# Optimization experiments

Measured on AMD Instinct MI355X. Metric: run time of the kernel, lower is better.

Reference implementation:

```python
import jax, jax.numpy as jnp
import numpy as np

B, T, C, H, DFF = 4, 1024, 1024, 16, 4096
HS = C // H  # 64
EPS = 1e-5


def layer_norm(x, g, b):
    mu = jnp.mean(x, axis=-1, keepdims=True)
    var = jnp.var(x, axis=-1, keepdims=True)
    return (x - mu) * jax.lax.rsqrt(var + EPS) * g + b


def setup_inputs() -> dict:
    key = jax.random.key(0)
    ks = jax.random.split(key, 12)
    s = 0.02
    return {
        "x": jax.random.normal(ks[0], (B, T, C), jnp.float32),
        "wq": jax.random.normal(ks[1], (H, C, HS), jnp.float32) * s,
        "wk": jax.random.normal(ks[2], (H, C, HS), jnp.float32) * s,
        "wv": jax.random.normal(ks[3], (H, C, HS), jnp.float32) * s,
        "w_proj": jax.random.normal(ks[4], (H * HS, C), jnp.float32) * s,
        "b_proj": jnp.zeros((C,), jnp.float32),
        "w1": jax.random.normal(ks[5], (C, DFF), jnp.float32) * s,
        "b1": jnp.zeros((DFF,), jnp.float32),
        "w2": jax.random.normal(ks[6], (DFF, C), jnp.float32) * s,
        "b2": jnp.zeros((C,), jnp.float32),
        "g1": jnp.ones((C,), jnp.float32),
        "be1": jnp.zeros((C,), jnp.float32),
        "g2": jnp.ones((C,), jnp.float32),
        "be2": jnp.zeros((C,), jnp.float32),
    }


def reference(x, wq, wk, wv, w_proj, b_proj, w1, b1, w2, b2, g1, be1, g2, be2):
    h = layer_norm(x, g1, be1)
    # per-head projections, vectorized over heads: [B,H,T,HS]
    q = jnp.einsum('btc,hcd->bhtd', h, wq)
    k = jnp.einsum('btc,hcd->bhtd', h, wk)
    v = jnp.einsum('btc,hcd->bhtd', h, wv)
    # mask=None in the original forward, so no causal masking
    wei = jnp.einsum('bhtd,bhsd->bhts', q, k) * (HS ** -0.5)
    wei = jax.nn.softmax(wei, axis=-1)  # [B,H,T,T]
    out = jnp.einsum('bhts,bhsd->bhtd', wei, v)
    out = out.transpose(0, 2, 1, 3).reshape(B, T, H * HS)  # concat heads
    attn_out = out @ w_proj + b_proj
    x = x + attn_out
    h2 = layer_norm(x, g2, be2)
    ff = jax.nn.relu(h2 @ w1 + b1) @ w2 + b2
    x = x + ff
    return x, wei
```

## Files before the change

kernel.cpp:

```cpp
#include <hip/hip_runtime.h>
#include <hip/hip_bf16.h>

#define BB    4
#define TT    1024
#define CC    1024
#define HH    16
#define HSZ   64
#define DFF   4096
#define NTOK  (BB*TT)
#define BHN   (BB*HH)

typedef __attribute__((ext_vector_type(8))) short bf16x8;
typedef __attribute__((ext_vector_type(4))) float f32x4;

__device__ __forceinline__ ushort f2b(float v) {
    union { float f; unsigned u; } c; c.f = v;
    unsigned r = c.u + 0x7fffu + ((c.u >> 16) & 1u);
    return (ushort)(r >> 16);
}
__device__ __forceinline__ void stv(float* p, float v)  { *p = v; }
__device__ __forceinline__ void stv(ushort* p, float v) { *p = f2b(v); }

__device__ __forceinline__ void gload16(const void* g, void* l) {
    __builtin_amdgcn_global_load_lds(
        (const __attribute__((address_space(1))) void*)g,
        (__attribute__((address_space(3))) void*)l, 16, 0, 0);
}

__global__ __launch_bounds__(256)
void ln_k(const float* __restrict__ x, const float* __restrict__ g,
          const float* __restrict__ be, ushort* __restrict__ o)
{
    __shared__ float s1[4], s2[4];
    long row = blockIdx.x;
    const float4* xr = (const float4*)(x + row * CC);
    float4 v = xr[threadIdx.x];
    float a = v.x + v.y + v.z + v.w;
    float b = v.x*v.x + v.y*v.y + v.z*v.z + v.w*v.w;
    for (int off = 32; off > 0; off >>= 1) {
        a += __shfl_down(a, off);
        b += __shfl_down(b, off);
    }
    if ((threadIdx.x & 63) == 0) { s1[threadIdx.x >> 6] = a; s2[threadIdx.x >> 6] = b; }
    __syncthreads();
    float sum = s1[0] + s1[1] + s1[2] + s1[3];
    float sq  = s2[0] + s2[1] + s2[2] + s2[3];
    float mu  = sum * (1.0f / CC);
    float var = sq * (1.0f / CC) - mu * mu;
    float inv = rsqrtf(var + 1e-5f);
    float4 gg = ((const float4*)g)[threadIdx.x];
    float4 bb = ((const float4*)be)[threadIdx.x];
    ushort4 r;
    r.x = f2b((v.x - mu) * inv * gg.x + bb.x);
    r.y = f2b((v.y - mu) * inv * gg.y + bb.y);
    r.z = f2b((v.z - mu) * inv * gg.z + bb.z);
    r.w = f2b((v.w - mu) * inv * gg.w + bb.w);
    ((ushort4*)(o + row * CC))[threadIdx.x] = r;
}

__global__ __launch_bounds__(256)
void tcvt_k(const float* __restrict__ src, ushort* __restrict__ dst, int R, int Cc)
{
    __shared__ float t[32][33];
    const long bz = blockIdx.z;
    src += bz * (long)R * Cc;
    dst += bz * (long)R * Cc;
    int r0 = blockIdx.y * 32, c0 = blockIdx.x * 32;
    int tx = threadIdx.x & 31, ty = threadIdx.x >> 5;
#pragma unroll
    for (int i = 0; i < 4; i++)
        t[ty + 8*i][tx] = src[(long)(r0 + ty + 8*i) * Cc + c0 + tx];
    __syncthreads();
#pragma unroll
    for (int i = 0; i < 4; i++)
        dst[(long)(c0 + ty + 8*i) * R + r0 + tx] = f2b(t[tx][ty + 8*i]);
}

enum { OL_PLAIN = 0, OL_QKV3 = 1 };
constexpr int EBIAS = 1, ERELU = 2, ERES = 4, ESCALE = 8;

template<int BM, int BN, int WM, int WN, int OL, int EPI, typename OutT>
__global__ __launch_bounds__(256)
void mgemm_k(const ushort* __restrict__ A, const ushort* __restrict__ Bt,
             const float* __restrict__ bias, const float* __restrict__ res,
             OutT* __restrict__ C, int M, int N, int K,
             long sA, long sB, long sC, float scale)
{
    constexpr int BK = 64;
    constexpr int FM = BM / WM / 16, FN = BN / WN / 16;
    __shared__ ushort As[BM * BK];
    __shared__ ushort Bs[BN * BK];
    const int tid = threadIdx.x;
    const int w = tid >> 6, l = tid & 63;
    const int wr = w / WN, wc = w % WN;
    const int l15 = l & 15, l4 = l >> 4;
    const int bh = blockIdx.z;
    const ushort* Ap = A  + (long)bh * sA + (long)(blockIdx.y * BM) * K;
    const ushort* Bp = Bt + (long)bh * sB + (long)(blockIdx.x * BN) * K;

    f32x4 acc[FM][FN];
#pragma unroll
    for (int m = 0; m < FM; m++)
#pragma unroll
        for (int n = 0; n < FN; n++) acc[m][n] = (f32x4){0.f, 0.f, 0.f, 0.f};

    const int arow = tid >> 3;
    const int achk = tid & 7;

    for (int k0 = 0; k0 < K; k0 += BK) {
#pragma unroll
        for (int i = 0; i < BM / 32; i++)
            gload16(Ap + (long)(i*32 + arow) * K + k0 + achk*8,
                    &As[(i*32 + w*8) * BK]);
#pragma unroll
        for (int i = 0; i < BN / 32; i++)
            gload16(Bp + (long)(i*32 + arow) * K + k0 + achk*8,
                    &Bs[(i*32 + w*8) * BK]);
        __syncthreads();
#pragma unroll
        for (int kk = 0; kk < 2; kk++) {
            const int ko = kk*32 + l4*8;
            bf16x8 af[FM], bfr[FN];
#pragma unroll
            for (int m = 0; m < FM; m++)
                af[m] = *(const bf16x8*)&As[(wr*(BM/WM) + m*16 + l15) * BK + ko];
#pragma unroll
            for (int n = 0; n < FN; n++)
                bfr[n] = *(const bf16x8*)&Bs[(wc*(BN/WN) + n*16 + l15) * BK + ko];
#pragma unroll
            for (int m = 0; m < FM; m++)
#pragma unroll
                for (int n = 0; n < FN; n++)
                    acc[m][n] = __builtin_amdgcn_mfma_f32_16x16x32_bf16(
                        af[m], bfr[n], acc[m][n], 0, 0, 0);
        }
        __syncthreads();
    }

#pragma unroll
    for (int m = 0; m < FM; m++) {
        int rbase = blockIdx.y*BM + wr*(BM/WM) + m*16 + l4*4;
#pragma unroll
        for (int n = 0; n < FN; n++) {
            int col = blockIdx.x*BN + wc*(BN/WN) + n*16 + l15;
#pragma unroll
            for (int r = 0; r < 4; r++) {
                int row = rbase + r;
                float v = acc[m][n][r];
                if (EPI & ESCALE) v *= scale;
                if (EPI & EBIAS)  v += bias[col];
                if (EPI & ERELU)  v = fmaxf(v, 0.f);
                if (EPI & ERES)   v += res[(long)row * N + col];
                long idx;
                if (OL == OL_PLAIN) {
                    idx = (long)row * N + col;
                } else {
                    int seg = col >> 10;
                    int cl  = col & 1023;
                    long bh_ = ((long)((row >> 10) * HH + (cl >> 6))) * 65536;
                    long off = (seg == 2)
                        ? bh_ + (long)(cl & 63) * 1024 + (row & 1023)
                        : bh_ + (long)(row & 1023) * 64 + (cl & 63);
                    idx = (long)seg * (4L << 20) + off;
                }
                stv(&C[(long)bh * sC + idx], v);
            }
        }
    }
}

__global__ __launch_bounds__(256, 2)
void fattn_k(const ushort* __restrict__ q_, const ushort* __restrict__ k_,
             const ushort* __restrict__ vt, float* __restrict__ wei,
             ushort* __restrict__ attn)
{
    __shared__ ushort Qs[128*64];
    __shared__ ushort Ks[128*64];
    __shared__ ushort Vs[64*128];
    __shared__ ushort Ps[128*128];
    float* sred = (float*)Ps;

    const int tid = threadIdx.x;
    const int w = tid >> 6, l = tid & 63;
    const int wr = w >> 1, wc = w & 1;
    const int l15 = l & 15, l4 = l >> 4;
    const int bh = blockIdx.y;
    const int q0 = blockIdx.x * 128;
    const int arow = tid >> 3, achk = tid & 7;

    const ushort* Qp = q_ + (long)bh * 65536;
    const ushort* Kp = k_ + (long)bh * 65536;
    const ushort* Vp = vt + (long)bh * 65536;

#pragma unroll
    for (int i = 0; i < 4; i++)
        gload16(Qp + (long)(q0 + i*32 + arow) * 64 + achk*8, &Qs[(i*32 + w*8)*64]);

    float ssum[4][4];
#pragma unroll
    for (int m = 0; m < 4; m++)
#pragma unroll
        for (int r = 0; r < 4; r++) ssum[m][r] = 0.f;

    for (int st = 0; st < 8; ++st) {
#pragma unroll
        for (int i = 0; i < 4; i++)
            gload16(Kp + (long)(st*128 + i*32 + arow) * 64 + achk*8,
                    &Ks[(i*32 + w*8)*64]);
        __syncthreads();

        f32x4 sacc[4][4];
#pragma unroll
        for (int m = 0; m < 4; m++)
#pragma unroll
            for (int n = 0; n < 4; n++) sacc[m][n] = (f32x4){0.f,0.f,0.f,0.f};
#pragma unroll
        for (int kk = 0; kk < 2; kk++) {
            const int ko = kk*32 + l4*8;
            bf16x8 af[4], bfr[4];
#pragma unroll
            for (int m = 0; m < 4; m++)
                af[m] = *(const bf16x8*)&Qs[(wr*64 + m*16 + l15)*64 + ko];
#pragma unroll
            for (int n = 0; n < 4; n++)
                bfr[n] = *(const bf16x8*)&Ks[(wc*64 + n*16 + l15)*64 + ko];
#pragma unroll
            for (int m = 0; m < 4; m++)
#pragma unroll
                for (int n = 0; n < 4; n++)
                    sacc[m][n] = __builtin_amdgcn_mfma_f32_16x16x32_bf16(
                        af[m], bfr[n], sacc[m][n], 0, 0, 0);
        }
#pragma unroll
        for (int m = 0; m < 4; m++)
#pragma unroll
            for (int r = 0; r < 4; r++) {
                float s = 0.f;
#pragma unroll
                for (int n = 0; n < 4; n++) s += __expf(sacc[m][n][r] * 0.125f);
                ssum[m][r] += s;
            }
        __syncthreads();
    }

    float linv[4][4];
#pragma unroll
    for (int m = 0; m < 4; m++)
#pragma unroll
        for (int r = 0; r < 4; r++) {
            float s = ssum[m][r];
#pragma unroll
            for (int d = 1; d < 16; d <<= 1) s += __shfl_xor(s, d);
            ssum[m][r] = s;
            if (l15 == 0) sred[wc*128 + wr*64 + m*16 + l4*4 + r] = s;
        }
    __syncthreads();
#pragma unroll
    for (int m = 0; m < 4; m++)
#pragma unroll
        for (int r = 0; r < 4; r++) {
            int rg = wr*64 + m*16 + l4*4 + r;
            linv[m][r] = 1.0f / (sred[rg] + sred[128 + rg]);
        }

    f32x4 oacc[4][2];
#pragma unroll
    for (int m = 0; m < 4; m++)
#pragma unroll
        for (int n = 0; n < 2; n++) oacc[m][n] = (f32x4){0.f,0.f,0.f,0.f};

    for (int st = 0; st < 8; ++st) {
#pragma unroll
        for (int i = 0; i < 4; i++)
            gload16(Kp + (long)(st*128 + i*32 + arow) * 64 + achk*8,
                    &Ks[(i*32 + w*8)*64]);
#pragma unroll
        for (int i = 0; i < 4; i++)
            gload16(Vp + (long)(i*16 + (tid>>4)) * 1024 + st*128 + (tid&15)*8,
                    &Vs[(i*16 + w*4)*128]);
        __syncthreads();

        f32x4 sacc[4][4];
#pragma unroll
        for (int m = 0; m < 4; m++)
#pragma unroll
            for (int n = 0; n < 4; n++) sacc[m][n] = (f32x4){0.f,0.f,0.f,0.f};
#pragma unroll
        for (int kk = 0; kk < 2; kk++) {
            const int ko = kk*32 + l4*8;
            bf16x8 af[4], bfr[4];
#pragma unroll
            for (int m = 0; m < 4; m++)
                af[m] = *(const bf16x8*)&Qs[(wr*64 + m*16 + l15)*64 + ko];
#pragma unroll
            for (int n = 0; n < 4; n++)
                bfr[n] = *(const bf16x8*)&Ks[(wc*64 + n*16 + l15)*64 + ko];
#pragma unroll
            for (int m = 0; m < 4; m++)
#pragma unroll
                for (int n = 0; n < 4; n++)
                    sacc[m][n] = __builtin_amdgcn_mfma_f32_16x16x32_bf16(
                        af[m], bfr[n], sacc[m][n], 0, 0, 0);
        }

        float* wrow = wei + (long)bh * (TT*(long)TT) + st*128;
#pragma unroll
        for (int m = 0; m < 4; m++)
#pragma unroll
            for (int r = 0; r < 4; r++) {
                int rg = wr*64 + m*16 + l4*4 + r;
                float li = linv[m][r];
#pragma unroll
                for (int n = 0; n < 4; n++) {
                    int col = wc*64 + n*16 + l15;
                    float p = __expf(sacc[m][n][r] * 0.125f) * li;
                    __builtin_nontemporal_store(p, &wrow[(long)(q0 + rg) * TT + col]);
                    Ps[rg*128 + col] = f2b(p);
                }
            }
        __syncthreads();

#pragma unroll
        for (int kc = 0; kc < 4; ++kc) {
            const int ko = kc*32 + l4*8;
            bf16x8 pa[4], vb[2];
#pragma unroll
            for (int m = 0; m < 4; m++)
                pa[m] = *(const bf16x8*)&Ps[(wr*64 + m*16 + l15)*128 + ko];
#pragma unroll
            for (int n = 0; n < 2; n++)
                vb[n] = *(const bf16x8*)&Vs[(wc*32 + n*16 + l15)*128 + ko];
#pragma unroll
            for (int m = 0; m < 4; m++)
#pragma unroll
                for (int n = 0; n < 2; n++)
                    oacc[m][n] = __builtin_amdgcn_mfma_f32_16x16x32_bf16(
                        pa[m], vb[n], oacc[m][n], 0, 0, 0);
        }
        __syncthreads();
    }

#pragma unroll
    for (int m = 0; m < 4; m++)
#pragma unroll
        for (int r = 0; r < 4; r++) {
            int rg = wr*64 + m*16 + l4*4 + r;
            long rowbase = ((long)(bh >> 4) * TT + q0 + rg) * CC + (long)(bh & 15) * HSZ;
#pragma unroll
            for (int n = 0; n < 2; n++)
                attn[rowbase + wc*32 + n*16 + l15] = f2b(oacc[m][n][r]);
        }
}

extern "C" void kernel_launch(void* const* d_in, const int* in_sizes, int n_in,
                              void* d_out, int out_size, void* d_ws, size_t ws_size,
                              hipStream_t stream)
{
    const float* x      = (const float*)d_in[0];
    const float* wq     = (const float*)d_in[1];
    const float* wk     = (const float*)d_in[2];
    const float* wv     = (const float*)d_in[3];
    const float* w_proj = (const float*)d_in[4];
    const float* b_proj = (const float*)d_in[5];
    const float* w1     = (const float*)d_in[6];
    const float* b1     = (const float*)d_in[7];
    const float* w2     = (const float*)d_in[8];
    const float* b2     = (const float*)d_in[9];
    const float* g1     = (const float*)d_in[10];
    const float* be1    = (const float*)d_in[11];
    const float* g2     = (const float*)d_in[12];
    const float* be2    = (const float*)d_in[13];

    float* out_x = (float*)d_out;
    float* wei   = out_x + (long)NTOK * CC;

    const long MEL = 1 << 20;
    ushort* ws16 = (ushort*)d_ws;
    ushort* h    = ws16;
    ushort* q_   = ws16 + 4*MEL;
    ushort* k_   = ws16 + 8*MEL;
    ushort* vt   = ws16 + 12*MEL;
    ushort* attn = ws16 + 16*MEL;
    ushort* h2   = ws16 + 20*MEL;
    ushort* a1   = ws16 + 24*MEL;
    ushort* wqkvT= ws16 + 40*MEL;
    ushort* w1T  = ws16 + 44*MEL;
    ushort* wpT  = ws16 + 48*MEL;
    ushort* w2T  = ws16 + 49*MEL;
    float*  x1   = (float*)(ws16 + 54*MEL);

    tcvt_k<<<dim3(2, 32, 16),  256, 0, stream>>>(wq,     wqkvT,           1024, 64);
    tcvt_k<<<dim3(2, 32, 16),  256, 0, stream>>>(wk,     wqkvT + 1*MEL,   1024, 64);
    tcvt_k<<<dim3(2, 32, 16),  256, 0, stream>>>(wv,     wqkvT + 2*MEL,   1024, 64);
    tcvt_k<<<dim3(32, 32, 1),  256, 0, stream>>>(w_proj, wpT, 1024, 1024);
    tcvt_k<<<dim3(128, 32, 1), 256, 0, stream>>>(w1,     w1T, 1024, 4096);
    tcvt_k<<<dim3(32, 128, 1), 256, 0, stream>>>(w2,     w2T, 4096, 1024);

    ln_k<<<NTOK, 256, 0, stream>>>(x, g1, be1, h);

    mgemm_k<128,128,2,2,OL_QKV3,0,ushort><<<dim3(24,32,1), 256, 0, stream>>>(
        h, wqkvT, nullptr, nullptr, q_, NTOK, 3072, CC, 0,0,0, 0.f);

    fattn_k<<<dim3(8, 64), 256, 0, stream>>>(q_, k_, vt, wei, attn);

    mgemm_k<128,128,2,2,OL_PLAIN,EBIAS|ERES,float><<<dim3(8,32,1), 256, 0, stream>>>(
        attn, wpT, b_proj, x, x1, NTOK, CC, CC, 0,0,0, 0.f);

    ln_k<<<NTOK, 256, 0, stream>>>(x1, g2, be2, h2);

    mgemm_k<128,128,2,2,OL_PLAIN,EBIAS|ERELU,ushort><<<dim3(32,32,1), 256, 0, stream>>>(
        h2, w1T, b1, nullptr, a1, NTOK, DFF, CC, 0,0,0, 0.f);

    mgemm_k<128,128,2,2,OL_PLAIN,EBIAS|ERES,float><<<dim3(8,32,1), 256, 0, stream>>>(
        a1, w2T, b2, x1, out_x, NTOK, CC, DFF, 0,0,0, 0.f);
}
```

Baseline: 393.7 us.

## Swizzle attention LDS tiles, add MFMA priority hints, merge weight conversions

Applies XOR swizzles to the Q, K, V and P shared-memory tiles in the attention kernel so the 16-byte MFMA fragment reads avoid LDS bank conflicts. It also raises wave priority around the MFMA loops and adds a barrier before P overwrites the reduction scratch. Separately, the six weight transpose/convert launches are merged into one kernel to cut launch overhead. The swizzle indexing must line up between the global-load writes and the fragment reads, which adds a risk of getting it wrong.

```diff
diff --git a/kernel.cpp b/kernel.cpp
--- a/kernel.cpp
+++ b/kernel.cpp
@@ -59,13 +59,32 @@
 }
 
 __global__ __launch_bounds__(256)
-void tcvt_k(const float* __restrict__ src, ushort* __restrict__ dst, int R, int Cc)
+void cvtall_k(const float* __restrict__ wq, const float* __restrict__ wk,
+              const float* __restrict__ wv, const float* __restrict__ wproj,
+              const float* __restrict__ w1, const float* __restrict__ w2,
+              ushort* __restrict__ wqkvT, ushort* __restrict__ wpT,
+              ushort* __restrict__ w1T, ushort* __restrict__ w2T)
 {
     __shared__ float t[32][33];
-    const long bz = blockIdx.z;
-    src += bz * (long)R * Cc;
-    dst += bz * (long)R * Cc;
-    int r0 = blockIdx.y * 32, c0 = blockIdx.x * 32;
+    int idx = blockIdx.x;
+    const float* src; ushort* dst; int R, Cc, bx, by;
+    if (idx < 3072) {
+        int seg = idx >> 10, rem = idx & 1023;
+        int z = rem >> 6, tt2 = rem & 63;
+        src = (seg == 0 ? wq : seg == 1 ? wk : wv) + (long)z * 65536;
+        dst = wqkvT + (long)seg * (1L << 20) + (long)z * 65536;
+        R = 1024; Cc = 64; bx = tt2 & 1; by = tt2 >> 1;
+    } else if (idx < 4096) {
+        int tt2 = idx - 3072;
+        src = wproj; dst = wpT; R = 1024; Cc = 1024; bx = tt2 & 31; by = tt2 >> 5;
+    } else if (idx < 8192) {
+        int tt2 = idx - 4096;
+        src = w1; dst = w1T; R = 1024; Cc = 4096; bx = tt2 & 127; by = tt2 >> 7;
+    } else {
+        int tt2 = idx - 8192;
+        src = w2; dst = w2T; R = 4096; Cc = 1024; bx = tt2 & 31; by = tt2 >> 5;
+    }
+    int r0 = by * 32, c0 = bx * 32;
     int tx = threadIdx.x & 31, ty = threadIdx.x >> 5;
 #pragma unroll
     for (int i = 0; i < 4; i++)
@@ -187,6 +206,11 @@
     const int bh = blockIdx.y;
     const int q0 = blockIdx.x * 128;
     const int arow = tid >> 3, achk = tid & 7;
+    const int kchk = achk ^ (arow & 7);
+    const int vrow = tid >> 4;
+    const int vchk = (tid & 15) ^ (vrow & 15);
+    const int sw8  = (l15 & 7) << 3;
+    const int sw16 = l15 << 3;
 
     const ushort* Qp = q_ + (long)bh * 65536;
     const ushort* Kp = k_ + (long)bh * 65536;
@@ -194,7 +218,7 @@
 
 #pragma unroll
     for (int i = 0; i < 4; i++)
-        gload16(Qp + (long)(q0 + i*32 + arow) * 64 + achk*8, &Qs[(i*32 + w*8)*64]);
+        gload16(Qp + (long)(q0 + i*32 + arow) * 64 + kchk*8, &Qs[(i*32 + w*8)*64]);
 
     float ssum[4][4];
 #pragma unroll
@@ -205,7 +229,7 @@
     for (int st = 0; st < 8; ++st) {
 #pragma unroll
         for (int i = 0; i < 4; i++)
-            gload16(Kp + (long)(st*128 + i*32 + arow) * 64 + achk*8,
+            gload16(Kp + (long)(st*128 + i*32 + arow) * 64 + kchk*8,
                     &Ks[(i*32 + w*8)*64]);
         __syncthreads();
 
@@ -214,16 +238,17 @@
         for (int m = 0; m < 4; m++)
 #pragma unroll
             for (int n = 0; n < 4; n++) sacc[m][n] = (f32x4){0.f,0.f,0.f,0.f};
+        __builtin_amdgcn_s_setprio(1);
 #pragma unroll
         for (int kk = 0; kk < 2; kk++) {
             const int ko = kk*32 + l4*8;
             bf16x8 af[4], bfr[4];
 #pragma unroll
             for (int m = 0; m < 4; m++)
-                af[m] = *(const bf16x8*)&Qs[(wr*64 + m*16 + l15)*64 + ko];
+                af[m] = *(const bf16x8*)&Qs[(wr*64 + m*16 + l15)*64 + (ko ^ sw8)];
 #pragma unroll
             for (int n = 0; n < 4; n++)
-                bfr[n] = *(const bf16x8*)&Ks[(wc*64 + n*16 + l15)*64 + ko];
+                bfr[n] = *(const bf16x8*)&Ks[(wc*64 + n*16 + l15)*64 + (ko ^ sw8)];
 #pragma unroll
             for (int m = 0; m < 4; m++)
 #pragma unroll
@@ -231,6 +256,7 @@
                     sacc[m][n] = __builtin_amdgcn_mfma_f32_16x16x32_bf16(
                         af[m], bfr[n], sacc[m][n], 0, 0, 0);
         }
+        __builtin_amdgcn_s_setprio(0);
 #pragma unroll
         for (int m = 0; m < 4; m++)
 #pragma unroll
@@ -262,6 +288,7 @@
             int rg = wr*64 + m*16 + l4*4 + r;
             linv[m][r] = 1.0f / (sred[rg] + sred[128 + rg]);
         }
+    __syncthreads();
 
     f32x4 oacc[4][2];
 #pragma unroll
@@ -272,11 +299,11 @@
     for (int st = 0; st < 8; ++st) {
 #pragma unroll
         for (int i = 0; i < 4; i++)
-            gload16(Kp + (long)(st*128 + i*32 + arow) * 64 + achk*8,
+            gload16(Kp + (long)(st*128 + i*32 + arow) * 64 + kchk*8,
                     &Ks[(i*32 + w*8)*64]);
 #pragma unroll
         for (int i = 0; i < 4; i++)
-            gload16(Vp + (long)(i*16 + (tid>>4)) * 1024 + st*128 + (tid&15)*8,
+            gload16(Vp + (long)(i*16 + vrow) * 1024 + st*128 + vchk*8,
                     &Vs[(i*16 + w*4)*128]);
         __syncthreads();
 
@@ -285,16 +312,17 @@
         for (int m = 0; m < 4; m++)
 #pragma unroll
             for (int n = 0; n < 4; n++) sacc[m][n] = (f32x4){0.f,0.f,0.f,0.f};
+        __builtin_amdgcn_s_setprio(1);
 #pragma unroll
         for (int kk = 0; kk < 2; kk++) {
             const int ko = kk*32 + l4*8;
             bf16x8 af[4], bfr[4];
 #pragma unroll
             for (int m = 0; m < 4; m++)
-                af[m] = *(const bf16x8*)&Qs[(wr*64 + m*16 + l15)*64 + ko];
+                af[m] = *(const bf16x8*)&Qs[(wr*64 + m*16 + l15)*64 + (ko ^ sw8)];
 #pragma unroll
             for (int n = 0; n < 4; n++)
-                bfr[n] = *(const bf16x8*)&Ks[(wc*64 + n*16 + l15)*64 + ko];
+                bfr[n] = *(const bf16x8*)&Ks[(wc*64 + n*16 + l15)*64 + (ko ^ sw8)];
 #pragma unroll
             for (int m = 0; m < 4; m++)
 #pragma unroll
@@ -302,6 +330,7 @@
                     sacc[m][n] = __builtin_amdgcn_mfma_f32_16x16x32_bf16(
                         af[m], bfr[n], sacc[m][n], 0, 0, 0);
         }
+        __builtin_amdgcn_s_setprio(0);
 
         float* wrow = wei + (long)bh * (TT*(long)TT) + st*128;
 #pragma unroll
@@ -309,27 +338,29 @@
 #pragma unroll
             for (int r = 0; r < 4; r++) {
                 int rg = wr*64 + m*16 + l4*4 + r;
+                int psw = (rg & 15) << 3;
                 float li = linv[m][r];
 #pragma unroll
                 for (int n = 0; n < 4; n++) {
                     int col = wc*64 + n*16 + l15;
                     float p = __expf(sacc[m][n][r] * 0.125f) * li;
                     __builtin_nontemporal_store(p, &wrow[(long)(q0 + rg) * TT + col]);
-                    Ps[rg*128 + col] = f2b(p);
+                    Ps[rg*128 + (col ^ psw)] = f2b(p);
                 }
             }
         __syncthreads();
 
+        __builtin_amdgcn_s_setprio(1);
 #pragma unroll
         for (int kc = 0; kc < 4; ++kc) {
             const int ko = kc*32 + l4*8;
             bf16x8 pa[4], vb[2];
 #pragma unroll
             for (int m = 0; m < 4; m++)
-                pa[m] = *(const bf16x8*)&Ps[(wr*64 + m*16 + l15)*128 + ko];
+                pa[m] = *(const bf16x8*)&Ps[(wr*64 + m*16 + l15)*128 + (ko ^ sw16)];
 #pragma unroll
             for (int n = 0; n < 2; n++)
-                vb[n] = *(const bf16x8*)&Vs[(wc*32 + n*16 + l15)*128 + ko];
+                vb[n] = *(const bf16x8*)&Vs[(wc*32 + n*16 + l15)*128 + (ko ^ sw16)];
 #pragma unroll
             for (int m = 0; m < 4; m++)
 #pragma unroll
@@ -337,6 +368,7 @@
                     oacc[m][n] = __builtin_amdgcn_mfma_f32_16x16x32_bf16(
                         pa[m], vb[n], oacc[m][n], 0, 0, 0);
         }
+        __builtin_amdgcn_s_setprio(0);
         __syncthreads();
     }
 
@@ -389,12 +421,8 @@
     ushort* w2T  = ws16 + 49*MEL;
     float*  x1   = (float*)(ws16 + 54*MEL);
 
-    tcvt_k<<<dim3(2, 32, 16),  256, 0, stream>>>(wq,     wqkvT,           1024, 64);
-    tcvt_k<<<dim3(2, 32, 16),  256, 0, stream>>>(wk,     wqkvT + 1*MEL,   1024, 64);
-    tcvt_k<<<dim3(2, 32, 16),  256, 0, stream>>>(wv,     wqkvT + 2*MEL,   1024, 64);
-    tcvt_k<<<dim3(32, 32, 1),  256, 0, stream>>>(w_proj, wpT, 1024, 1024);
-    tcvt_k<<<dim3(128, 32, 1), 256, 0, stream>>>(w1,     w1T, 1024, 4096);
-    tcvt_k<<<dim3(32, 128, 1), 256, 0, stream>>>(w2,     w2T, 4096, 1024);
+    cvtall_k<<<12288, 256, 0, stream>>>(wq, wk, wv, w_proj, w1, w2,
+                                        wqkvT, wpT, w1T, w2T);
 
     ln_k<<<NTOK, 256, 0, stream>>>(x, g1, be1, h);
 
```

Result: faster. 381.3 us (-3.2%).
